# Kernel tuning notes

Hardware: AMD Instinct MI355X
Metric: run time of the kernel (lower is better)

## Reference

```python
import jax, jax.numpy as jnp
import numpy as np

D_MODEL = 1024
N_HEADS = 16
D_K = D_MODEL // N_HEADS
THETA = 10000.0
B, S = 2, 2048


def _rope(x):
    # x: [B, H, S, Dh], interleaved-pair RoPE with positions arange(S)
    Dh = x.shape[-1]
    inv_freq = 1.0 / (THETA ** (jnp.arange(0, Dh, 2, dtype=jnp.float32) / Dh))  # [Dh/2]
    pos = jnp.arange(x.shape[-2], dtype=jnp.float32)
    ang = pos[:, None] * inv_freq[None, :]                      # [S, Dh/2]
    cos = jnp.repeat(jnp.cos(ang), 2, axis=-1).astype(x.dtype)  # [S, Dh]
    sin = jnp.repeat(jnp.sin(ang), 2, axis=-1).astype(x.dtype)
    # rotate pairs: (x_2k, x_2k+1) -> (-x_2k+1, x_2k)
    xp = x.reshape(*x.shape[:-1], Dh // 2, 2)
    rot = jnp.stack((-xp[..., 1], xp[..., 0]), axis=-1).reshape(x.shape)
    return x * cos + rot * sin


def setup_inputs() -> dict:
    key = jax.random.key(0)
    ks = jax.random.split(key, 5)
    std = (2.0 / (D_MODEL + D_MODEL)) ** 0.5
    return {
        "x": jax.random.normal(ks[0], (B, S, D_MODEL), dtype=jnp.float32),
        "wq": jax.random.normal(ks[1], (D_MODEL, D_MODEL), dtype=jnp.float32) * std,
        "wk": jax.random.normal(ks[2], (D_MODEL, D_MODEL), dtype=jnp.float32) * std,
        "wv": jax.random.normal(ks[3], (D_MODEL, D_MODEL), dtype=jnp.float32) * std,
        "wo": jax.random.normal(ks[4], (D_MODEL, D_MODEL), dtype=jnp.float32) * std,
    }


def reference(x, wq, wk, wv, wo):
    b, s, _ = x.shape
    def split_heads(t):
        return t.reshape(b, s, N_HEADS, D_K).transpose(0, 2, 1, 3)  # [B,H,S,Dk]
    # Linear: y = x @ W.T  (weights stored [out, in])
    q = split_heads(jnp.einsum('bsd,od->bso', x, wq))
    k = split_heads(jnp.einsum('bsd,od->bso', x, wk))
    v = split_heads(jnp.einsum('bsd,od->bso', x, wv))
    q = _rope(q)
    k = _rope(k)
    scores = jnp.einsum('bhqd,bhkd->bhqk', q, k) / jnp.sqrt(jnp.asarray(D_K, x.dtype))
    causal = jnp.tril(jnp.ones((s, s), dtype=bool))
    scores = jnp.where(causal[None, None], scores, -jnp.inf)
    attn = jax.nn.softmax(scores, axis=-1)
    out = jnp.einsum('bhqk,bhkd->bhqd', attn, v)
    out = out.transpose(0, 2, 1, 3).reshape(b, s, D_MODEL)
    return jnp.einsum('bsd,od->bso', out, wo)
```

## Files before the change

### kernel.cpp

```cpp
#include <hip/hip_runtime.h>


typedef unsigned short u16;
typedef __attribute__((ext_vector_type(8))) short short8;
typedef __attribute__((ext_vector_type(4))) float float4v;

#define LSTR 72
#define QSCL 0.18033688011112042f

__device__ __forceinline__ u16 f2b(float f) {
    union { float f; unsigned int i; } t; t.f = f;
    unsigned int r = t.i + 0x7fffu + ((t.i >> 16) & 1u);
    return (u16)(r >> 16);
}

__global__ __launch_bounds__(256) void cvt_all(
    const float4* __restrict__ x,  const float4* __restrict__ wq,
    const float4* __restrict__ wk, const float4* __restrict__ wv,
    const float4* __restrict__ wo,
    u16* __restrict__ xb, u16* __restrict__ wcat, u16* __restrict__ wob)
{
    const int i = blockIdx.x * 256 + threadIdx.x;
    const float4* s; u16* d; int off;
    if (i < 524288) { s = x; d = xb; off = i; }
    else {
        const int widx = i - 524288;
        const int w = widx >> 17, o = widx & 131071;
        switch (w) {
            case 0:  s = wq; d = wcat;              break;
            case 1:  s = wk; d = wcat + (1 << 20);  break;
            case 2:  s = wv; d = wcat + (2 << 20);  break;
            default: s = wo; d = wob;               break;
        }
        off = o;
    }
    float4 a = s[2 * off], b = s[2 * off + 1];
    u16 t[8] = {f2b(a.x), f2b(a.y), f2b(a.z), f2b(a.w),
                f2b(b.x), f2b(b.y), f2b(b.z), f2b(b.w)};
    reinterpret_cast<int4*>(d)[off] = *reinterpret_cast<int4*>(t);
}

__global__ __launch_bounds__(256) void gemm128(
    const u16* __restrict__ X, const u16* __restrict__ Wb,
    u16* __restrict__ Yq, u16* __restrict__ Yk, u16* __restrict__ Yv,
    float* __restrict__ Yf, int rope)
{
    __shared__ u16 As[128 * LSTR];
    __shared__ u16 Bs[128 * LSTR];

    const int tid  = threadIdx.x;
    const int wave = tid >> 6;
    const int lane = tid & 63;
    const int quad = lane >> 4;
    const int l16  = lane & 15;
    const int wm = (wave >> 1) * 64, wn = (wave & 1) * 64;
    const int m0 = blockIdx.y * 128, n0 = blockIdx.x * 128;
    const int srow = tid >> 1;
    const int cb   = (tid & 1) * 32;

    float4v acc[4][4];
#pragma unroll
    for (int mt = 0; mt < 4; mt++)
#pragma unroll
        for (int nt = 0; nt < 4; nt++) acc[mt][nt] = (float4v){0.f, 0.f, 0.f, 0.f};

    int4 a0, a1, a2, a3, b0, b1, b2, b3;
    {
        const int4* gA = reinterpret_cast<const int4*>(X + (size_t)(m0 + srow) * 1024 + cb);
        a0 = gA[0]; a1 = gA[1]; a2 = gA[2]; a3 = gA[3];
        const int4* gB = reinterpret_cast<const int4*>(Wb + (size_t)(n0 + srow) * 1024 + cb);
        b0 = gB[0]; b1 = gB[1]; b2 = gB[2]; b3 = gB[3];
    }

    for (int kb = 0; kb < 1024; kb += 64) {
        __syncthreads();
        *reinterpret_cast<int4*>(&As[srow * LSTR + cb])      = a0;
        *reinterpret_cast<int4*>(&As[srow * LSTR + cb + 8])  = a1;
        *reinterpret_cast<int4*>(&As[srow * LSTR + cb + 16]) = a2;
        *reinterpret_cast<int4*>(&As[srow * LSTR + cb + 24]) = a3;
        *reinterpret_cast<int4*>(&Bs[srow * LSTR + cb])      = b0;
        *reinterpret_cast<int4*>(&Bs[srow * LSTR + cb + 8])  = b1;
        *reinterpret_cast<int4*>(&Bs[srow * LSTR + cb + 16]) = b2;
        *reinterpret_cast<int4*>(&Bs[srow * LSTR + cb + 24]) = b3;
        __syncthreads();
        if (kb + 64 < 1024) {
            const int4* gA = reinterpret_cast<const int4*>(X + (size_t)(m0 + srow) * 1024 + kb + 64 + cb);
            a0 = gA[0]; a1 = gA[1]; a2 = gA[2]; a3 = gA[3];
            const int4* gB = reinterpret_cast<const int4*>(Wb + (size_t)(n0 + srow) * 1024 + kb + 64 + cb);
            b0 = gB[0]; b1 = gB[1]; b2 = gB[2]; b3 = gB[3];
        }
#pragma unroll
        for (int ks = 0; ks < 2; ks++) {
            short8 af[4], bf[4];
#pragma unroll
            for (int t = 0; t < 4; t++) {
                af[t] = *reinterpret_cast<const short8*>(&As[(wm + t * 16 + l16) * LSTR + ks * 32 + quad * 8]);
                bf[t] = *reinterpret_cast<const short8*>(&Bs[(wn + t * 16 + l16) * LSTR + ks * 32 + quad * 8]);
            }
#pragma unroll
            for (int mt = 0; mt < 4; mt++)
#pragma unroll
                for (int nt = 0; nt < 4; nt++)
                    acc[mt][nt] = __builtin_amdgcn_mfma_f32_16x16x32_bf16(af[mt], bf[nt], acc[mt][nt], 0, 0, 0);
        }
    }

    if (rope) {
#pragma unroll
        for (int nt = 0; nt < 4; nt++) {
            const int cg = n0 + wn + nt * 16 + l16;
            const int buf = cg >> 10;
            const int c = cg & 1023;
            u16* dst = (buf == 0) ? Yq : ((buf == 1) ? Yk : Yv);
            const bool rp = (buf < 2);
            const float scl = (buf == 0) ? QSCL : 1.0f;
            float freq = 0.f;
            if (rp) freq = exp2f((float)((cg & 63) >> 1) * -0.4152410118609203f);
#pragma unroll
            for (int mt = 0; mt < 4; mt++)
#pragma unroll
                for (int r = 0; r < 4; r++) {
                    const int row = m0 + wm + mt * 16 + quad * 4 + r;
                    float v = acc[mt][nt][r];
                    if (rp) {
                        float sn, cs; sincosf((float)(row & 2047) * freq, &sn, &cs);
                        const float partner = __shfl_xor(v, 1);
                        v = (l16 & 1) ? fmaf(v, cs,  partner * sn)
                                      : fmaf(v, cs, -partner * sn);
                    }
                    dst[(size_t)row * 1024 + c] = f2b(v * scl);
                }
        }
    } else {
#pragma unroll
        for (int nt = 0; nt < 4; nt++) {
            const int col = n0 + wn + nt * 16 + l16;
#pragma unroll
            for (int mt = 0; mt < 4; mt++)
#pragma unroll
                for (int r = 0; r < 4; r++) {
                    const int row = m0 + wm + mt * 16 + quad * 4 + r;
                    Yf[(size_t)row * 1024 + col] = acc[mt][nt][r];
                }
        }
    }
}

__global__ __launch_bounds__(256, 2) void attn_kernel(
    const u16* Q, const u16* __restrict__ K,
    const u16* __restrict__ V, u16* O)
{
    __shared__ u16 Vt[64 * LSTR];
    __shared__ u16 Ps[4 * 16 * LSTR];

    const int tid  = threadIdx.x;
    const int wave = tid >> 6;
    const int lane = tid & 63;
    const int quad = lane >> 4;
    const int l16  = lane & 15;
    const int qtA = blockIdx.x;
    const int qtB = 31 - qtA;
    const int h = blockIdx.y, b = blockIdx.z;
    const size_t base = ((size_t)b * 2048) * 1024 + (size_t)h * 64;

    short8 qfA[2], qfB[2];
    {
        const size_t ra = base + (size_t)(qtA * 64 + wave * 16 + l16) * 1024;
        qfA[0] = *reinterpret_cast<const short8*>(Q + ra + quad * 8);
        qfA[1] = *reinterpret_cast<const short8*>(Q + ra + 32 + quad * 8);
        const size_t rb = base + (size_t)(qtB * 64 + wave * 16 + l16) * 1024;
        qfB[0] = *reinterpret_cast<const short8*>(Q + rb + quad * 8);
        qfB[1] = *reinterpret_cast<const short8*>(Q + rb + 32 + quad * 8);
    }

    float4v oA[4], oB[4];
#pragma unroll
    for (int i = 0; i < 4; i++) { oA[i] = (float4v){0.f,0.f,0.f,0.f}; oB[i] = (float4v){0.f,0.f,0.f,0.f}; }
    float sA[4] = {0.f,0.f,0.f,0.f}, sB[4] = {0.f,0.f,0.f,0.f};

    u16* Pw = Ps + wave * 16 * LSTR;
    const int srow = tid >> 2;
    const int cb   = (tid & 3) << 4;
    const int sxw  = srow ^ cb;

    const u16* Vp = V + base + (size_t)srow * 1024 + cb;
    const u16* kbase = K + base + (size_t)l16 * 1024 + quad * 8;
    int4 vr0 = *reinterpret_cast<const int4*>(Vp), vr1 = *reinterpret_cast<const int4*>(Vp + 8);
    short8 kn[4][2], kc[4][2], vf[4][2];
#pragma unroll
    for (int nt = 0; nt < 4; nt++)
#pragma unroll
        for (int ks = 0; ks < 2; ks++)
            kn[nt][ks] = *reinterpret_cast<const short8*>(kbase + (size_t)(nt * 16) * 1024 + ks * 32);

    auto proc = [&](const short8 (&qf)[2], float4v (&oc)[4], float (&sr)[4], bool diag) {
        float4v sacc[4];
#pragma unroll
        for (int nt = 0; nt < 4; nt++) {
            sacc[nt] = (float4v){0.f, 0.f, 0.f, 0.f};
#pragma unroll
            for (int ks = 0; ks < 2; ks++)
                sacc[nt] = __builtin_amdgcn_mfma_f32_16x16x32_bf16(qf[ks], kc[nt][ks], sacc[nt], 0, 0, 0);
        }
#pragma unroll
        for (int r = 0; r < 4; r++) {
            const int qloc = wave * 16 + quad * 4 + r;
#pragma unroll
            for (int nt = 0; nt < 4; nt++) {
                float s = sacc[nt][r];
                if (diag && (nt * 16 + l16 > qloc)) s = -1e30f;
                const float p = exp2f(s);
                sr[r] += p;
                Pw[(quad * 4 + r) * LSTR + nt * 16 + l16] = f2b(p);
            }
        }
        __builtin_amdgcn_wave_barrier();
#pragma unroll
        for (int ks = 0; ks < 2; ks++) {
            short8 pf = *reinterpret_cast<const short8*>(&Pw[l16 * LSTR + ks * 32 + quad * 8]);
#pragma unroll
            for (int dt = 0; dt < 4; dt++)
                oc[dt] = __builtin_amdgcn_mfma_f32_16x16x32_bf16(pf, vf[dt][ks], oc[dt], 0, 0, 0);
        }
        __builtin_amdgcn_wave_barrier();
    };

    for (int j = 0; j <= qtB; j++) {
        __syncthreads();
        {
            const u16* a = reinterpret_cast<const u16*>(&vr0);
            const u16* c = reinterpret_cast<const u16*>(&vr1);
#pragma unroll
            for (int e = 0; e < 8; e++) Vt[(cb + e) * LSTR + sxw] = a[e];
#pragma unroll
            for (int e = 0; e < 8; e++) Vt[(cb + 8 + e) * LSTR + sxw] = c[e];
        }
#pragma unroll
        for (int nt = 0; nt < 4; nt++)
#pragma unroll
            for (int ks = 0; ks < 2; ks++) kc[nt][ks] = kn[nt][ks];
        __syncthreads();
        if (j < qtB) {
            Vp += 65536;
            vr0 = *reinterpret_cast<const int4*>(Vp); vr1 = *reinterpret_cast<const int4*>(Vp + 8);
            const u16* kb2 = kbase + (size_t)(j + 1) * 65536;
#pragma unroll
            for (int nt = 0; nt < 4; nt++)
#pragma unroll
                for (int ks = 0; ks < 2; ks++)
                    kn[nt][ks] = *reinterpret_cast<const short8*>(kb2 + (size_t)(nt * 16) * 1024 + ks * 32);
        }
#pragma unroll
        for (int nt = 0; nt < 4; nt++)
#pragma unroll
            for (int ks = 0; ks < 2; ks++)
                vf[nt][ks] = *reinterpret_cast<const short8*>(&Vt[(nt * 16 + l16) * LSTR + ((ks * 32 + quad * 8) ^ (nt << 4))]);
        if (j <= qtA) proc(qfA, oA, sA, j == qtA);
        proc(qfB, oB, sB, j == qtB);
    }

#pragma unroll
    for (int r = 0; r < 4; r++) {
        float la = sA[r], lb = sB[r];
#pragma unroll
        for (int msk = 1; msk < 16; msk <<= 1) { la += __shfl_xor(la, msk); lb += __shfl_xor(lb, msk); }
        const float invA = 1.0f / la, invB = 1.0f / lb;
        const int rloc = wave * 16 + quad * 4 + r;
        const size_t rowA = base + (size_t)(qtA * 64 + rloc) * 1024;
        const size_t rowB = base + (size_t)(qtB * 64 + rloc) * 1024;
#pragma unroll
        for (int dt = 0; dt < 4; dt++) {
            O[rowA + dt * 16 + l16] = f2b(oA[dt][r] * invA);
            O[rowB + dt * 16 + l16] = f2b(oB[dt][r] * invB);
        }
    }
}

extern "C" void kernel_launch(void* const* d_in, const int* in_sizes, int n_in,
                              void* d_out, int out_size, void* d_ws, size_t ws_size,
                              hipStream_t stream) {
    (void)in_sizes; (void)n_in; (void)out_size; (void)ws_size;
    const float* x  = (const float*)d_in[0];
    const float* wq = (const float*)d_in[1];
    const float* wk = (const float*)d_in[2];
    const float* wv = (const float*)d_in[3];
    const float* wo = (const float*)d_in[4];

    const size_t MN = (size_t)4096 * 1024;

    u16* xb   = (u16*)d_out;
    u16* wcat = xb + MN;
    u16* qbuf = (u16*)d_ws;
    u16* kbuf = qbuf + MN;
    u16* vbuf = kbuf + MN;
    u16* wob  = vbuf + MN;

    cvt_all<<<4096, 256, 0, stream>>>((const float4*)x, (const float4*)wq,
                                      (const float4*)wk, (const float4*)wv,
                                      (const float4*)wo, xb, wcat, wob);
    gemm128<<<dim3(24, 32), 256, 0, stream>>>(xb, wcat, qbuf, kbuf, vbuf, nullptr, 1);
    attn_kernel<<<dim3(16, 16, 2), 256, 0, stream>>>(qbuf, kbuf, vbuf, qbuf);
    gemm128<<<dim3(8, 32), 256, 0, stream>>>(qbuf, wob, nullptr, nullptr, nullptr, (float*)d_out, 0);
}
```

Before: 228.7 us.

## Use direct global-to-LDS loads with XOR swizzle and remap GEMM tiles

Result: slower. 243.2 us (+6.3%).

```diff
diff --git a/kernel.cpp b/kernel.cpp
--- a/kernel.cpp
+++ b/kernel.cpp
@@ -5,7 +5,10 @@
 typedef __attribute__((ext_vector_type(8))) short short8;
 typedef __attribute__((ext_vector_type(4))) float float4v;
 
-#define LSTR 72
+typedef const __attribute__((address_space(1))) void GV;
+typedef __attribute__((address_space(3))) void LV;
+
+#define VSTR 72
 #define QSCL 0.18033688011112042f
 
 __device__ __forceinline__ u16 f2b(float f) {
@@ -40,74 +43,70 @@
     reinterpret_cast<int4*>(d)[off] = *reinterpret_cast<int4*>(t);
 }
 
-__global__ __launch_bounds__(256) void gemm128(
+template<int NT, int ROPE, int NBLK>
+__global__ __launch_bounds__(256) void gemm_tile(
     const u16* __restrict__ X, const u16* __restrict__ Wb,
     u16* __restrict__ Yq, u16* __restrict__ Yk, u16* __restrict__ Yv,
-    float* __restrict__ Yf, int rope)
+    float* __restrict__ Yf)
 {
-    __shared__ u16 As[128 * LSTR];
-    __shared__ u16 Bs[128 * LSTR];
+    __shared__ u16 As[128 * 64];
+    __shared__ u16 Bs[NT * 32 * 64];
 
     const int tid  = threadIdx.x;
     const int wave = tid >> 6;
     const int lane = tid & 63;
     const int quad = lane >> 4;
     const int l16  = lane & 15;
-    const int wm = (wave >> 1) * 64, wn = (wave & 1) * 64;
-    const int m0 = blockIdx.y * 128, n0 = blockIdx.x * 128;
-    const int srow = tid >> 1;
-    const int cb   = (tid & 1) * 32;
-
-    float4v acc[4][4];
+    const int wm = (wave >> 1) * 64, wn = (wave & 1) * (NT * 16);
+    const int g = blockIdx.x;
+    const int rr = g >> 3;
+    const int m0 = ((g & 7) * 4 + rr / NBLK) * 128;
+    const int n0 = (rr % NBLK) * (NT * 32);
+    const int lrow = lane >> 3;
+    const int cg8  = (lane & 7) ^ lrow;
+
+    float4v acc[4][NT];
 #pragma unroll
     for (int mt = 0; mt < 4; mt++)
 #pragma unroll
-        for (int nt = 0; nt < 4; nt++) acc[mt][nt] = (float4v){0.f, 0.f, 0.f, 0.f};
-
-    int4 a0, a1, a2, a3, b0, b1, b2, b3;
-    {
-        const int4* gA = reinterpret_cast<const int4*>(X + (size_t)(m0 + srow) * 1024 + cb);
-        a0 = gA[0]; a1 = gA[1]; a2 = gA[2]; a3 = gA[3];
-        const int4* gB = reinterpret_cast<const int4*>(Wb + (size_t)(n0 + srow) * 1024 + cb);
-        b0 = gB[0]; b1 = gB[1]; b2 = gB[2]; b3 = gB[3];
-    }
+        for (int nt = 0; nt < NT; nt++) acc[mt][nt] = (float4v){0.f, 0.f, 0.f, 0.f};
 
     for (int kb = 0; kb < 1024; kb += 64) {
         __syncthreads();
-        *reinterpret_cast<int4*>(&As[srow * LSTR + cb])      = a0;
-        *reinterpret_cast<int4*>(&As[srow * LSTR + cb + 8])  = a1;
-        *reinterpret_cast<int4*>(&As[srow * LSTR + cb + 16]) = a2;
-        *reinterpret_cast<int4*>(&As[srow * LSTR + cb + 24]) = a3;
-        *reinterpret_cast<int4*>(&Bs[srow * LSTR + cb])      = b0;
-        *reinterpret_cast<int4*>(&Bs[srow * LSTR + cb + 8])  = b1;
-        *reinterpret_cast<int4*>(&Bs[srow * LSTR + cb + 16]) = b2;
-        *reinterpret_cast<int4*>(&Bs[srow * LSTR + cb + 24]) = b3;
+#pragma unroll
+        for (int t = 0; t < 4; t++) {
+            const int I = wave * 4 + t;
+            const u16* gp = X + (size_t)(m0 + I * 8 + lrow) * 1024 + kb + cg8 * 8;
+            __builtin_amdgcn_global_load_lds((GV*)gp, (LV*)&As[I * 512], 16, 0, 0);
+        }
+#pragma unroll
+        for (int t = 0; t < NT; t++) {
+            const int I = wave * NT + t;
+            const u16* gp = Wb + (size_t)(n0 + I * 8 + lrow) * 1024 + kb + cg8 * 8;
+            __builtin_amdgcn_global_load_lds((GV*)gp, (LV*)&Bs[I * 512], 16, 0, 0);
+        }
         __syncthreads();
-        if (kb + 64 < 1024) {
-            const int4* gA = reinterpret_cast<const int4*>(X + (size_t)(m0 + srow) * 1024 + kb + 64 + cb);
-            a0 = gA[0]; a1 = gA[1]; a2 = gA[2]; a3 = gA[3];
-            const int4* gB = reinterpret_cast<const int4*>(Wb + (size_t)(n0 + srow) * 1024 + kb + 64 + cb);
-            b0 = gB[0]; b1 = gB[1]; b2 = gB[2]; b3 = gB[3];
-        }
 #pragma unroll
         for (int ks = 0; ks < 2; ks++) {
-            short8 af[4], bf[4];
-#pragma unroll
-            for (int t = 0; t < 4; t++) {
-                af[t] = *reinterpret_cast<const short8*>(&As[(wm + t * 16 + l16) * LSTR + ks * 32 + quad * 8]);
-                bf[t] = *reinterpret_cast<const short8*>(&Bs[(wn + t * 16 + l16) * LSTR + ks * 32 + quad * 8]);
-            }
+            const int su = ((ks * 4 + quad) ^ (l16 & 7)) * 8;
+            short8 af[4], bf[NT];
+#pragma unroll
+            for (int t = 0; t < 4; t++)
+                af[t] = *reinterpret_cast<const short8*>(&As[(wm + t * 16 + l16) * 64 + su]);
+#pragma unroll
+            for (int t = 0; t < NT; t++)
+                bf[t] = *reinterpret_cast<const short8*>(&Bs[(wn + t * 16 + l16) * 64 + su]);
 #pragma unroll
             for (int mt = 0; mt < 4; mt++)
 #pragma unroll
-                for (int nt = 0; nt < 4; nt++)
+                for (int nt = 0; nt < NT; nt++)
                     acc[mt][nt] = __builtin_amdgcn_mfma_f32_16x16x32_bf16(af[mt], bf[nt], acc[mt][nt], 0, 0, 0);
         }
     }
 
-    if (rope) {
-#pragma unroll
-        for (int nt = 0; nt < 4; nt++) {
+    if (ROPE) {
+#pragma unroll
+        for (int nt = 0; nt < NT; nt++) {
             const int cg = n0 + wn + nt * 16 + l16;
             const int buf = cg >> 10;
             const int c = cg & 1023;
@@ -133,7 +132,7 @@
         }
     } else {
 #pragma unroll
-        for (int nt = 0; nt < 4; nt++) {
+        for (int nt = 0; nt < NT; nt++) {
             const int col = n0 + wn + nt * 16 + l16;
 #pragma unroll
             for (int mt = 0; mt < 4; mt++)
@@ -150,8 +149,8 @@
     const u16* Q, const u16* __restrict__ K,
     const u16* __restrict__ V, u16* O)
 {
-    __shared__ u16 Vt[64 * LSTR];
-    __shared__ u16 Ps[4 * 16 * LSTR];
+    __shared__ u16 Vt[64 * VSTR];
+    __shared__ u16 Ps[4 * 16 * VSTR];
 
     const int tid  = threadIdx.x;
     const int wave = tid >> 6;
@@ -178,14 +177,14 @@
     for (int i = 0; i < 4; i++) { oA[i] = (float4v){0.f,0.f,0.f,0.f}; oB[i] = (float4v){0.f,0.f,0.f,0.f}; }
     float sA[4] = {0.f,0.f,0.f,0.f}, sB[4] = {0.f,0.f,0.f,0.f};
 
-    u16* Pw = Ps + wave * 16 * LSTR;
-    const int srow = tid >> 2;
-    const int cb   = (tid & 3) << 4;
-    const int sxw  = srow ^ cb;
-
-    const u16* Vp = V + base + (size_t)srow * 1024 + cb;
+    u16* Pw = Ps + wave * 16 * VSTR;
+    const int s0 = (tid & 31) * 2;
+    const int d0 = (tid >> 5) * 8;
+
+    const u16* Vp = V + base + (size_t)s0 * 1024 + d0;
     const u16* kbase = K + base + (size_t)l16 * 1024 + quad * 8;
-    int4 vr0 = *reinterpret_cast<const int4*>(Vp), vr1 = *reinterpret_cast<const int4*>(Vp + 8);
+    int4 vr0 = *reinterpret_cast<const int4*>(Vp);
+    int4 vr1 = *reinterpret_cast<const int4*>(Vp + 1024);
     short8 kn[4][2], kc[4][2], vf[4][2];
 #pragma unroll
     for (int nt = 0; nt < 4; nt++)
@@ -211,13 +210,13 @@
                 if (diag && (nt * 16 + l16 > qloc)) s = -1e30f;
                 const float p = exp2f(s);
                 sr[r] += p;
-                Pw[(quad * 4 + r) * LSTR + nt * 16 + l16] = f2b(p);
+                Pw[(quad * 4 + r) * VSTR + nt * 16 + l16] = f2b(p);
             }
         }
         __builtin_amdgcn_wave_barrier();
 #pragma unroll
         for (int ks = 0; ks < 2; ks++) {
-            short8 pf = *reinterpret_cast<const short8*>(&Pw[l16 * LSTR + ks * 32 + quad * 8]);
+            short8 pf = *reinterpret_cast<const short8*>(&Pw[l16 * VSTR + ks * 32 + quad * 8]);
 #pragma unroll
             for (int dt = 0; dt < 4; dt++)
                 oc[dt] = __builtin_amdgcn_mfma_f32_16x16x32_bf16(pf, vf[dt][ks], oc[dt], 0, 0, 0);
@@ -231,9 +230,10 @@
             const u16* a = reinterpret_cast<const u16*>(&vr0);
             const u16* c = reinterpret_cast<const u16*>(&vr1);
 #pragma unroll
-            for (int e = 0; e < 8; e++) Vt[(cb + e) * LSTR + sxw] = a[e];
-#pragma unroll
-            for (int e = 0; e < 8; e++) Vt[(cb + 8 + e) * LSTR + sxw] = c[e];
+            for (int e = 0; e < 8; e++) {
+                const unsigned int pk = (unsigned int)a[e] | ((unsigned int)c[e] << 16);
+                *reinterpret_cast<unsigned int*>(&Vt[(d0 + e) * VSTR + s0]) = pk;
+            }
         }
 #pragma unroll
         for (int nt = 0; nt < 4; nt++)
@@ -242,7 +242,8 @@
         __syncthreads();
         if (j < qtB) {
             Vp += 65536;
-            vr0 = *reinterpret_cast<const int4*>(Vp); vr1 = *reinterpret_cast<const int4*>(Vp + 8);
+            vr0 = *reinterpret_cast<const int4*>(Vp);
+            vr1 = *reinterpret_cast<const int4*>(Vp + 1024);
             const u16* kb2 = kbase + (size_t)(j + 1) * 65536;
 #pragma unroll
             for (int nt = 0; nt < 4; nt++)
@@ -254,7 +255,7 @@
         for (int nt = 0; nt < 4; nt++)
 #pragma unroll
             for (int ks = 0; ks < 2; ks++)
-                vf[nt][ks] = *reinterpret_cast<const short8*>(&Vt[(nt * 16 + l16) * LSTR + ((ks * 32 + quad * 8) ^ (nt << 4))]);
+                vf[nt][ks] = *reinterpret_cast<const short8*>(&Vt[(nt * 16 + l16) * VSTR + ks * 32 + quad * 8]);
         if (j <= qtA) proc(qfA, oA, sA, j == qtA);
         proc(qfB, oB, sB, j == qtB);
     }
@@ -298,7 +299,7 @@
     cvt_all<<<4096, 256, 0, stream>>>((const float4*)x, (const float4*)wq,
                                       (const float4*)wk, (const float4*)wv,
                                       (const float4*)wo, xb, wcat, wob);
-    gemm128<<<dim3(24, 32), 256, 0, stream>>>(xb, wcat, qbuf, kbuf, vbuf, nullptr, 1);
+    gemm_tile<4, 1, 24><<<768, 256, 0, stream>>>(xb, wcat, qbuf, kbuf, vbuf, nullptr);
     attn_kernel<<<dim3(16, 16, 2), 256, 0, stream>>>(qbuf, kbuf, vbuf, qbuf);
-    gemm128<<<dim3(8, 32), 256, 0, stream>>>(qbuf, wob, nullptr, nullptr, nullptr, (float*)d_out, 0);
-}
+    gemm_tile<2, 0, 16><<<512, 256, 0, stream>>>(qbuf, wob, nullptr, nullptr, nullptr, (float*)d_out);
+}
```
